# Kernel optimization log

Hardware: AMD Instinct MI355X
Metric: run time of the kernel (lower is better)

Reference implementation:

```python
import jax, jax.numpy as jnp
import numpy as np

NB, NA, NC, NH, NW = 128, 5, 80, 28, 28
NT = 50
ANCHORS = jnp.array([2.8, 4.8, 5.1, 10.2, 6.4, 16.3, 9.2, 19.8, 14.1, 23.7], dtype=jnp.float32)
ANCHOR_W = ANCHORS[0::2]  # [NA]
ANCHOR_H = ANCHORS[1::2]
OBJECT_SCALE = 5.0
NOOBJECT_SCALE = 1.0
CLASS_SCALE = 1.0
COORD_SCALE = 1.0
SIL_THRESH = 0.6


def iou_cxcywh(b1, b2):
    # center-format IoU, matches bbox_ious(x1y1x2y2=False); inputs broadcastable (...,4)
    x1, y1, w1, h1 = b1[..., 0], b1[..., 1], b1[..., 2], b1[..., 3]
    x2, y2, w2, h2 = b2[..., 0], b2[..., 1], b2[..., 2], b2[..., 3]
    mx = jnp.minimum(x1 - w1 / 2, x2 - w2 / 2)
    Mx = jnp.maximum(x1 + w1 / 2, x2 + w2 / 2)
    my = jnp.minimum(y1 - h1 / 2, y2 - h2 / 2)
    My = jnp.maximum(y1 + h1 / 2, y2 + h2 / 2)
    cw = w1 + w2 - (Mx - mx)
    ch = h1 + h2 - (My - my)
    inter = jnp.where((cw > 0) & (ch > 0), cw * ch, 0.0)
    union = w1 * h1 + w2 * h2 - inter
    return inter / union


def build_targets(pred_boxes, target):
    # pred_boxes: [NB, NA, NH, NW, 4] grid-unit cxcywh (already detached)
    tgt = target.reshape(NB, NT, 5)
    gcls = tgt[..., 0]
    gx = tgt[..., 1] * NW
    gy = tgt[..., 2] * NH
    gw = tgt[..., 3] * NW
    gh = tgt[..., 4] * NH
    gt_boxes = jnp.stack([gx, gy, gw, gh], -1)  # [NB, NT, 4]

    # silence mask: any-GT IoU > thresh -> conf_mask 0, else noobject_scale
    pb = pred_boxes.reshape(NB, NA * NH * NW, 4)
    ious = iou_cxcywh(pb[:, :, None, :], gt_boxes[:, None, :, :])  # [NB, nAnchors, NT]
    max_iou = jnp.max(ious, axis=2)
    conf_mask0 = jnp.where(max_iou > SIL_THRESH, 0.0, NOOBJECT_SCALE).reshape(NB, NA, NH, NW)

    # best anchor per GT by wh-only IoU at origin
    z_na = jnp.zeros((NA,), jnp.float32)
    anc = jnp.stack([z_na, z_na, ANCHOR_W, ANCHOR_H], -1)  # [NA,4]
    zg = jnp.zeros_like(gw)
    gt_wh = jnp.stack([zg, zg, gw, gh], -1)  # [NB,NT,4]
    a_iou = iou_cxcywh(gt_wh[:, :, None, :], anc[None, None, :, :])  # [NB,NT,NA]
    best_n = jnp.argmax(a_iou, axis=2)  # [NB,NT] (first max, matches strict > loop)

    gi = jnp.floor(gx).astype(jnp.int32)
    gj = jnp.floor(gy).astype(jnp.int32)
    flat_idx = ((jnp.arange(NB)[:, None] * NA + best_n) * NH + gj) * NW + gi  # [NB,NT]

    assigned_pred = pred_boxes.reshape(NB * NA * NH * NW, 4)[flat_idx]  # [NB,NT,4]
    iou_gt_pred = iou_cxcywh(gt_boxes, assigned_pred)  # [NB,NT]
    aw = ANCHOR_W[best_n]
    ah = ANCHOR_H[best_n]

    idx = flat_idx.reshape(-1)
    grid0 = jnp.zeros((NB * NA * NH * NW,), jnp.float32)

    def sc(init_flat, v):
        return init_flat.at[idx].set(v.reshape(-1)).reshape(NB, NA, NH, NW)

    ones = jnp.ones((NB, NT), jnp.float32)
    coord_mask = sc(grid0, ones)
    cls_mask = sc(grid0, ones)
    conf_mask = sc(conf_mask0.reshape(-1), jnp.full((NB, NT), OBJECT_SCALE, jnp.float32))
    tx = sc(grid0, gx - gi.astype(jnp.float32))
    ty = sc(grid0, gy - gj.astype(jnp.float32))
    tw = sc(grid0, jnp.log(gw / aw))
    th = sc(grid0, jnp.log(gh / ah))
    tconf = sc(grid0, iou_gt_pred)
    tcls = sc(grid0, gcls)
    return coord_mask, conf_mask, cls_mask, tx, ty, tw, th, tconf, tcls


def _smooth_l1_sum(a, b):
    d = a - b
    ad = jnp.abs(d)
    return jnp.sum(jnp.where(ad < 1.0, 0.5 * d * d, ad - 0.5))


def _forward(output, target):
    out = output.reshape(NB, NA, 5 + NC, NH, NW)
    x = jax.nn.sigmoid(out[:, :, 0])
    y = jax.nn.sigmoid(out[:, :, 1])
    w = out[:, :, 2]
    h = out[:, :, 3]
    conf = jax.nn.sigmoid(out[:, :, 4])
    cls_logits = jnp.transpose(out[:, :, 5:], (0, 1, 3, 4, 2))  # [NB,NA,NH,NW,NC]

    gx = jnp.arange(NW, dtype=jnp.float32)[None, None, None, :]
    gy = jnp.arange(NH, dtype=jnp.float32)[None, None, :, None]
    sg = jax.lax.stop_gradient
    px = sg(x) + gx
    py = sg(y) + gy
    pw = jnp.exp(sg(w)) * ANCHOR_W[None, :, None, None]
    ph = jnp.exp(sg(h)) * ANCHOR_H[None, :, None, None]
    pred_boxes = jnp.stack([px, py, pw, ph], -1)  # [NB,NA,NH,NW,4]

    bt = jax.lax.stop_gradient(build_targets(pred_boxes, target))
    coord_mask, conf_mask, cls_mask, tx, ty, tw, th, tconf, tcls = bt
    conf_mask = jnp.sqrt(conf_mask)

    loss_x = COORD_SCALE * _smooth_l1_sum(x * coord_mask, tx * coord_mask) / 2.0
    loss_y = COORD_SCALE * _smooth_l1_sum(y * coord_mask, ty * coord_mask) / 2.0
    loss_w = COORD_SCALE * _smooth_l1_sum(w * coord_mask, tw * coord_mask) / 2.0
    loss_h = COORD_SCALE * _smooth_l1_sum(h * coord_mask, th * coord_mask) / 2.0
    loss_conf = jnp.sum((conf * conf_mask - tconf * conf_mask) ** 2) / 2.0

    # focal loss (gamma=2, alpha=1, sum reduction) over cells with cls_mask==1
    logp = jax.nn.log_softmax(cls_logits, axis=-1)
    logp_t = jnp.take_along_axis(logp, tcls[..., None].astype(jnp.int32), axis=-1)[..., 0]
    p_t = jnp.exp(logp_t)
    focal = -((1.0 - p_t) ** 2) * logp_t
    loss_cls = CLASS_SCALE * jnp.sum(cls_mask * focal)

    return loss_x + loss_y + loss_w + loss_h + loss_conf + loss_cls


def setup_inputs() -> dict:
    key = jax.random.key(0)
    k1, k2, k3 = jax.random.split(key, 3)
    output = jax.random.normal(k1, (NB, NA * (5 + NC), NH, NW), dtype=jnp.float32)
    u = jax.random.uniform(k2, (NB, NT, 4), dtype=jnp.float32)
    xy = 0.1 + 0.8 * u[..., :2]   # x in (0.1,0.9) -> never 0, no early break
    wh = 0.05 + 0.45 * u[..., 2:]
    cls_id = jax.random.randint(k3, (NB, NT, 1), 0, NC).astype(jnp.float32)
    target = jnp.concatenate([cls_id, xy, wh], axis=-1).reshape(NB, NT * 5)
    return {"output": output, "target": target}


def reference(output, target):
    return _forward(output, target)
```

## Files before the change

kernel.cpp:

```cpp
#include <hip/hip_runtime.h>
#include <math.h>

#define NBB 128
#define NAA 5
#define NCC 80
#define NHH 28
#define NWW 28
#define NTT 50
#define CH  85
#define HW  784
#define CELLS 3920
#define NREC  6400

__constant__ float c_AW[5] = {2.8f, 5.1f, 6.4f, 9.2f, 14.1f};
__constant__ float c_AH[5] = {4.8f, 10.2f, 16.3f, 19.8f, 23.7f};

__device__ __forceinline__ float sigmoidf_(float x) {
    return 1.0f / (1.0f + __expf(-x));
}

__device__ __forceinline__ float smooth_l1(float d) {
    float ad = fabsf(d);
    return (ad < 1.0f) ? 0.5f * d * d : ad - 0.5f;
}

__global__ __launch_bounds__(64) void prep_targets(
    const float* __restrict__ out, const float* __restrict__ tgt,
    int* __restrict__ recIdx, float* __restrict__ recF)
{
    const int b = blockIdx.x;
    const int t = threadIdx.x;
    __shared__ int cellS[64];

    int   cell = -1;
    float tx = 0.f, ty = 0.f, tw = 0.f, th = 0.f, tconf = 0.f, tcls = 0.f;

    if (t < NTT) {
        const float* tp = tgt + b * NTT * 5 + t * 5;
        float cls = tp[0];
        float gx = tp[1] * NWW;
        float gy = tp[2] * NHH;
        float gw = tp[3] * NWW;
        float gh = tp[4] * NHH;
        float ga = gw * gh;

        int best = 0; float bestI = -1.0f;
        for (int a = 0; a < 5; ++a) {
            float inter = fminf(gw, c_AW[a]) * fminf(gh, c_AH[a]);
            float uni   = ga + c_AW[a] * c_AH[a] - inter;
            float iou   = inter / uni;
            if (iou > bestI) { bestI = iou; best = a; }
        }
        int gi = (int)floorf(gx);
        int gj = (int)floorf(gy);
        cell = (best * NHH + gj) * NWW + gi;

        const float* op = out + ((size_t)(b * NAA + best) * CH) * HW + gj * NWW + gi;
        float px = sigmoidf_(op[0])      + (float)gi;
        float py = sigmoidf_(op[HW])     + (float)gj;
        float pw = __expf(op[2 * HW]) * c_AW[best];
        float ph = __expf(op[3 * HW]) * c_AH[best];

        float mx = fminf(px - pw * 0.5f, gx - gw * 0.5f);
        float Mx = fmaxf(px + pw * 0.5f, gx + gw * 0.5f);
        float my = fminf(py - ph * 0.5f, gy - gh * 0.5f);
        float My = fmaxf(py + ph * 0.5f, gy + gh * 0.5f);
        float cw  = pw + gw - (Mx - mx);
        float chh = ph + gh - (My - my);
        float inter = (cw > 0.f && chh > 0.f) ? cw * chh : 0.f;
        float uni   = pw * ph + ga - inter;

        tconf = inter / uni;
        tx = gx - (float)gi;
        ty = gy - (float)gj;
        tw = __logf(gw / c_AW[best]);
        th = __logf(gh / c_AH[best]);
        tcls = cls;
    }

    cellS[t] = cell;
    __syncthreads();

    if (t < NTT) {
        bool active = true;
        for (int t2 = t + 1; t2 < NTT; ++t2)
            if (cellS[t2] == cell) active = false;
        int r = b * NTT + t;
        recIdx[r]            = active ? cell : -1;
        recF[0 * NREC + r] = tx;
        recF[1 * NREC + r] = ty;
        recF[2 * NREC + r] = tw;
        recF[3 * NREC + r] = th;
        recF[4 * NREC + r] = tconf;
        recF[5 * NREC + r] = tcls;
    }
}

__global__ __launch_bounds__(256) void conf_loss(
    const float* __restrict__ out, const float* __restrict__ tgt,
    const int* __restrict__ recIdx, const float* __restrict__ recTconf,
    float* __restrict__ d_out)
{
    __shared__ float L2[NTT], R2[NTT], T2[NTT], B2[NTT], AR[NTT];
    __shared__ int   rIdx[NTT];
    __shared__ float rTc[NTT];
    __shared__ float red[256];

    const int b   = blockIdx.y;
    const int tid = threadIdx.x;

    if (tid < NTT) {
        const float* tp = tgt + b * NTT * 5 + tid * 5;
        float gx = tp[1] * NWW, gy = tp[2] * NHH;
        float gw = tp[3] * NWW, gh = tp[4] * NHH;
        L2[tid] = gx - gw * 0.5f;
        R2[tid] = gx + gw * 0.5f;
        T2[tid] = gy - gh * 0.5f;
        B2[tid] = gy + gh * 0.5f;
        AR[tid] = gw * gh;
    } else if (tid >= 64 && tid < 64 + NTT) {
        int j = tid - 64;
        rIdx[j] = recIdx[b * NTT + j];
        rTc[j]  = recTconf[b * NTT + j];
    }
    __syncthreads();

    const int cell = blockIdx.x * 256 + tid;
    float term = 0.0f;

    if (cell < CELLS) {
        int a  = cell / HW;
        int hw = cell - a * HW;
        int wi = hw % NWW;
        int hj = hw / NWW;
        const float* op = out + ((size_t)(b * NAA + a) * CH) * HW + hw;

        float px   = sigmoidf_(op[0])  + (float)wi;
        float py   = sigmoidf_(op[HW]) + (float)hj;
        float pw   = __expf(op[2 * HW]) * c_AW[a];
        float ph   = __expf(op[3 * HW]) * c_AH[a];
        float conf = sigmoidf_(op[4 * HW]);

        float l1 = px - pw * 0.5f, r1 = px + pw * 0.5f;
        float t1 = py - ph * 0.5f, b1 = py + ph * 0.5f;
        float a1 = pw * ph;

        bool flag = false;
        #pragma unroll 5
        for (int j = 0; j < NTT; ++j) {
            float cw  = fminf(r1, R2[j]) - fmaxf(l1, L2[j]);
            float chh = fminf(b1, B2[j]) - fmaxf(t1, T2[j]);
            float inter = (cw > 0.f && chh > 0.f) ? cw * chh : 0.f;
            flag = flag || (inter * 1.6f > 0.6f * (a1 + AR[j]));
        }

        bool assigned = false; float tc = 0.f;
        for (int j = 0; j < NTT; ++j) {
            if (rIdx[j] == cell) { assigned = true; tc = rTc[j]; }
        }

        if (assigned) { float d = conf - tc; term = 2.5f * d * d; }
        else if (!flag) { term = 0.5f * conf * conf; }
    }

    red[tid] = term;
    __syncthreads();
    for (int s = 128; s > 0; s >>= 1) {
        if (tid < s) red[tid] += red[tid + s];
        __syncthreads();
    }
    if (tid == 0) atomicAdd(d_out, red[0]);
}

__global__ __launch_bounds__(64) void assigned_loss(
    const float* __restrict__ out, const int* __restrict__ recIdx,
    const float* __restrict__ recF, float* __restrict__ d_out)
{
    const int lane = threadIdx.x;
    float acc = 0.0f;

    for (int k = 0; k < 4; ++k) {
        int r = blockIdx.x * 4 + k;
        int cell = recIdx[r];
        if (cell < 0) continue;
        int b  = r / NTT;
        int a  = cell / HW;
        int hw = cell - a * HW;
        const float* op = out + ((size_t)(b * NAA + a) * CH) * HW + hw;

        float l0 = op[(5 + lane) * HW];
        float l1 = (lane < 16) ? op[(5 + 64 + lane) * HW] : -INFINITY;

        float m = fmaxf(l0, l1);
        for (int o = 32; o >= 1; o >>= 1) m = fmaxf(m, __shfl_xor(m, o));
        float s = __expf(l0 - m) + ((lane < 16) ? __expf(l1 - m) : 0.0f);
        for (int o = 32; o >= 1; o >>= 1) s += __shfl_xor(s, o);

        int t = (int)recF[5 * NREC + r];
        float lt = (t < 64) ? __shfl(l0, t) : __shfl(l1, t - 64);
        float logpt = lt - m - __logf(s);
        float pt = __expf(logpt);
        float focal = -(1.0f - pt) * (1.0f - pt) * logpt;

        if (lane == 0) {
            float tx = recF[0 * NREC + r];
            float ty = recF[1 * NREC + r];
            float tw = recF[2 * NREC + r];
            float th = recF[3 * NREC + r];
            float x = sigmoidf_(op[0]);
            float y = sigmoidf_(op[HW]);
            float w = op[2 * HW];
            float h = op[3 * HW];
            acc += focal;
            acc += 0.5f * (smooth_l1(x - tx) + smooth_l1(y - ty) +
                           smooth_l1(w - tw) + smooth_l1(h - th));
        }
    }
    if (lane == 0) atomicAdd(d_out, acc);
}

extern "C" void kernel_launch(void* const* d_in, const int* in_sizes, int n_in,
                              void* d_out, int out_size, void* d_ws, size_t ws_size,
                              hipStream_t stream) {
    const float* out_p = (const float*)d_in[0];
    const float* tgt_p = (const float*)d_in[1];
    float* loss = (float*)d_out;

    int*   recIdx = (int*)d_ws;
    float* recF   = (float*)d_ws + NREC;

    hipMemsetAsync(loss, 0, (size_t)out_size * sizeof(float), stream);

    prep_targets<<<dim3(NBB), dim3(64), 0, stream>>>(out_p, tgt_p, recIdx, recF);
    conf_loss<<<dim3(16, NBB), dim3(256), 0, stream>>>(out_p, tgt_p, recIdx,
                                                       recF + 4 * NREC, loss);
    assigned_loss<<<dim3(NREC / 4), dim3(64), 0, stream>>>(out_p, recIdx, recF, loss);
}
```

Baseline: 272.2 us.

## Fuse target prep into conf loss kernel and parallelize assigned loss per wave

Target preparation now runs inside each conf-loss block, which recomputes the per-image GT boxes, best-anchor cells and tconf in shared memory. This removes one kernel launch and the dependency on a global record buffer between the two stages. Only blockIdx.x==0 writes the records needed by the assigned-loss kernel, which now runs one record per wave with 4 waves per block instead of a serial loop over 4 records. The cost is 16x redundant prep work (including a gather from the output tensor) per image, plus an extra shared-memory reduction in the assigned kernel.

```diff
diff --git a/kernel.cpp b/kernel.cpp
--- a/kernel.cpp
+++ b/kernel.cpp
@@ -24,19 +24,23 @@
     return (ad < 1.0f) ? 0.5f * d * d : ad - 0.5f;
 }
 
-__global__ __launch_bounds__(64) void prep_targets(
+__global__ __launch_bounds__(256) void prep_conf_loss(
     const float* __restrict__ out, const float* __restrict__ tgt,
-    int* __restrict__ recIdx, float* __restrict__ recF)
+    int* __restrict__ recIdx, float* __restrict__ recF,
+    float* __restrict__ d_out)
 {
-    const int b = blockIdx.x;
-    const int t = threadIdx.x;
-    __shared__ int cellS[64];
-
-    int   cell = -1;
-    float tx = 0.f, ty = 0.f, tw = 0.f, th = 0.f, tconf = 0.f, tcls = 0.f;
-
-    if (t < NTT) {
-        const float* tp = tgt + b * NTT * 5 + t * 5;
+    __shared__ float L2[NTT], R2[NTT], T2[NTT], B2[NTT], AR[NTT];
+    __shared__ int   rCell[NTT];
+    __shared__ float rTc[NTT];
+    __shared__ float red[256];
+
+    const int b   = blockIdx.y;
+    const int tid = threadIdx.x;
+
+    float tx = 0.f, ty = 0.f, tw = 0.f, th = 0.f, tcls = 0.f;
+
+    if (tid < NTT) {
+        const float* tp = tgt + b * NTT * 5 + tid * 5;
         float cls = tp[0];
         float gx = tp[1] * NWW;
         float gy = tp[2] * NHH;
@@ -44,7 +48,14 @@
         float gh = tp[4] * NHH;
         float ga = gw * gh;
 
+        L2[tid] = gx - gw * 0.5f;
+        R2[tid] = gx + gw * 0.5f;
+        T2[tid] = gy - gh * 0.5f;
+        B2[tid] = gy + gh * 0.5f;
+        AR[tid] = ga;
+
         int best = 0; float bestI = -1.0f;
+        #pragma unroll
         for (int a = 0; a < 5; ++a) {
             float inter = fminf(gw, c_AW[a]) * fminf(gh, c_AH[a]);
             float uni   = ga + c_AW[a] * c_AH[a] - inter;
@@ -53,7 +64,7 @@
         }
         int gi = (int)floorf(gx);
         int gj = (int)floorf(gy);
-        cell = (best * NHH + gj) * NWW + gi;
+        int cell = (best * NHH + gj) * NWW + gi;
 
         const float* op = out + ((size_t)(b * NAA + best) * CH) * HW + gj * NWW + gi;
         float px = sigmoidf_(op[0])      + (float)gi;
@@ -70,60 +81,30 @@
         float inter = (cw > 0.f && chh > 0.f) ? cw * chh : 0.f;
         float uni   = pw * ph + ga - inter;
 
-        tconf = inter / uni;
+        rCell[tid] = cell;
+        rTc[tid]   = inter / uni;
+
         tx = gx - (float)gi;
         ty = gy - (float)gj;
         tw = __logf(gw / c_AW[best]);
         th = __logf(gh / c_AH[best]);
         tcls = cls;
     }
-
-    cellS[t] = cell;
     __syncthreads();
 
-    if (t < NTT) {
+    if (blockIdx.x == 0 && tid < NTT) {
+        int cell = rCell[tid];
         bool active = true;
-        for (int t2 = t + 1; t2 < NTT; ++t2)
-            if (cellS[t2] == cell) active = false;
-        int r = b * NTT + t;
-        recIdx[r]            = active ? cell : -1;
+        for (int t2 = tid + 1; t2 < NTT; ++t2)
+            if (rCell[t2] == cell) active = false;
+        int r = b * NTT + tid;
+        recIdx[r]          = active ? cell : -1;
         recF[0 * NREC + r] = tx;
         recF[1 * NREC + r] = ty;
         recF[2 * NREC + r] = tw;
         recF[3 * NREC + r] = th;
-        recF[4 * NREC + r] = tconf;
-        recF[5 * NREC + r] = tcls;
-    }
-}
-
-__global__ __launch_bounds__(256) void conf_loss(
-    const float* __restrict__ out, const float* __restrict__ tgt,
-    const int* __restrict__ recIdx, const float* __restrict__ recTconf,
-    float* __restrict__ d_out)
-{
-    __shared__ float L2[NTT], R2[NTT], T2[NTT], B2[NTT], AR[NTT];
-    __shared__ int   rIdx[NTT];
-    __shared__ float rTc[NTT];
-    __shared__ float red[256];
-
-    const int b   = blockIdx.y;
-    const int tid = threadIdx.x;
-
-    if (tid < NTT) {
-        const float* tp = tgt + b * NTT * 5 + tid * 5;
-        float gx = tp[1] * NWW, gy = tp[2] * NHH;
-        float gw = tp[3] * NWW, gh = tp[4] * NHH;
-        L2[tid] = gx - gw * 0.5f;
-        R2[tid] = gx + gw * 0.5f;
-        T2[tid] = gy - gh * 0.5f;
-        B2[tid] = gy + gh * 0.5f;
-        AR[tid] = gw * gh;
-    } else if (tid >= 64 && tid < 64 + NTT) {
-        int j = tid - 64;
-        rIdx[j] = recIdx[b * NTT + j];
-        rTc[j]  = recTconf[b * NTT + j];
-    }
-    __syncthreads();
+        recF[4 * NREC + r] = tcls;
+    }
 
     const int cell = blockIdx.x * 256 + tid;
     float term = 0.0f;
@@ -156,7 +137,7 @@
 
         bool assigned = false; float tc = 0.f;
         for (int j = 0; j < NTT; ++j) {
-            if (rIdx[j] == cell) { assigned = true; tc = rTc[j]; }
+            if (rCell[j] == cell) { assigned = true; tc = rTc[j]; }
         }
 
         if (assigned) { float d = conf - tc; term = 2.5f * d * d; }
@@ -172,17 +153,19 @@
     if (tid == 0) atomicAdd(d_out, red[0]);
 }
 
-__global__ __launch_bounds__(64) void assigned_loss(
+__global__ __launch_bounds__(256) void assigned_loss(
     const float* __restrict__ out, const int* __restrict__ recIdx,
     const float* __restrict__ recF, float* __restrict__ d_out)
 {
-    const int lane = threadIdx.x;
-    float acc = 0.0f;
-
-    for (int k = 0; k < 4; ++k) {
-        int r = blockIdx.x * 4 + k;
-        int cell = recIdx[r];
-        if (cell < 0) continue;
+    const int wave = threadIdx.x >> 6;
+    const int lane = threadIdx.x & 63;
+    const int r    = blockIdx.x * 4 + wave;
+
+    __shared__ float ws[4];
+    float contrib = 0.0f;
+
+    int cell = recIdx[r];
+    if (cell >= 0) {
         int b  = r / NTT;
         int a  = cell / HW;
         int hw = cell - a * HW;
@@ -196,7 +179,7 @@
         float s = __expf(l0 - m) + ((lane < 16) ? __expf(l1 - m) : 0.0f);
         for (int o = 32; o >= 1; o >>= 1) s += __shfl_xor(s, o);
 
-        int t = (int)recF[5 * NREC + r];
+        int t = (int)recF[4 * NREC + r];
         float lt = (t < 64) ? __shfl(l0, t) : __shfl(l1, t - 64);
         float logpt = lt - m - __logf(s);
         float pt = __expf(logpt);
@@ -211,12 +194,16 @@
             float y = sigmoidf_(op[HW]);
             float w = op[2 * HW];
             float h = op[3 * HW];
-            acc += focal;
-            acc += 0.5f * (smooth_l1(x - tx) + smooth_l1(y - ty) +
-                           smooth_l1(w - tw) + smooth_l1(h - th));
-        }
-    }
-    if (lane == 0) atomicAdd(d_out, acc);
+            contrib = focal +
+                      0.5f * (smooth_l1(x - tx) + smooth_l1(y - ty) +
+                              smooth_l1(w - tw) + smooth_l1(h - th));
+        }
+    }
+
+    if (lane == 0) ws[wave] = contrib;
+    __syncthreads();
+    if (threadIdx.x == 0)
+        atomicAdd(d_out, ws[0] + ws[1] + ws[2] + ws[3]);
 }
 
 extern "C" void kernel_launch(void* const* d_in, const int* in_sizes, int n_in,
@@ -231,8 +218,8 @@
 
     hipMemsetAsync(loss, 0, (size_t)out_size * sizeof(float), stream);
 
-    prep_targets<<<dim3(NBB), dim3(64), 0, stream>>>(out_p, tgt_p, recIdx, recF);
-    conf_loss<<<dim3(16, NBB), dim3(256), 0, stream>>>(out_p, tgt_p, recIdx,
-                                                       recF + 4 * NREC, loss);
-    assigned_loss<<<dim3(NREC / 4), dim3(64), 0, stream>>>(out_p, recIdx, recF, loss);
-}
+    prep_conf_loss<<<dim3(16, NBB), dim3(256), 0, stream>>>(
+        out_p, tgt_p, recIdx, recF, loss);
+    assigned_loss<<<dim3(NREC / 4), dim3(256), 0, stream>>>(
+        out_p, recIdx, recF, loss);
+}
```

Result: no change. 267.5 us (-1.7%).
